# Performance work log

Measured on AMD Instinct MI355X. Metric: run time of the kernel, lower is better.

The kernel has to match this reference:

```python
import math
import jax, jax.numpy as jnp
import numpy as np

N_SENSORS = 4760
K = 16
HID = 64
D_LAT = 1024
D_PROJ = 128
POS_DIM = 96
FACE_DIM = 32
OUT_CH = 1
N_HEADS = 4
HEAD_DIM = D_PROJ // N_HEADS
N_TOKENS = 6
NUM_BANDS = POS_DIM // 6
B = 16


def _sinusoidal_pos_encoding(positions, num_bands):
    # positions: (N,3) numpy -> (N, num_bands*2*3)
    freq = (2.0 ** np.arange(num_bands, dtype=np.float32))
    encs = []
    for d in range(3):
        scaled = positions[:, d:d + 1] * freq[None, :] * (math.pi / 100.0)
        encs.append(np.sin(scaled))
        encs.append(np.cos(scaled))
    return np.concatenate(encs, axis=-1).astype(np.float32)


def setup_inputs() -> dict:
    rng = np.random.default_rng(0)
    positions = rng.uniform(-100.0, 100.0, (N_SENSORS, 3)).astype(np.float32)
    # kNN graph by 3D euclidean distance
    d2 = ((positions[:, None, :] - positions[None, :, :]) ** 2).sum(-1)
    knn = np.argsort(d2, axis=1)[:, :K].astype(np.int32)
    face_ids = rng.integers(0, 6, N_SENSORS).astype(np.int32)
    pos_embed = _sinusoidal_pos_encoding(positions, NUM_BANDS)  # (N,96)

    key = jax.random.key(0)
    ks = jax.random.split(key, 20)
    def lin(k, din, dout):
        k1, k2 = jax.random.split(k)
        lim = 1.0 / math.sqrt(din)
        W = jax.random.uniform(k1, (din, dout), jnp.float32, -lim, lim)
        b = jax.random.uniform(k2, (dout,), jnp.float32, -lim, lim)
        return W, b

    W_nbr, b_nbr = lin(ks[0], 2 + POS_DIM + FACE_DIM, HID)
    W_ql, b_ql = lin(ks[1], POS_DIM + FACE_DIM, HID)
    W_lat, b_lat = lin(ks[2], D_LAT, D_PROJ)
    W_lf, b_lf = lin(ks[3], FACE_DIM, D_PROJ)
    W_qg, b_qg = lin(ks[4], POS_DIM + FACE_DIM, D_PROJ)
    W_k, b_k = lin(ks[5], D_PROJ, D_PROJ)
    W_v, b_v = lin(ks[6], D_PROJ, D_PROJ)
    W_go, b_go = lin(ks[7], D_PROJ, D_PROJ)
    W_m1, b_m1 = lin(ks[8], HID + D_PROJ, HID)
    W_m2, b_m2 = lin(ks[9], HID, OUT_CH)
    face_emb = jax.random.normal(ks[10], (6, FACE_DIM), jnp.float32)
    ln_g = jnp.ones((HID + D_PROJ,), jnp.float32)
    ln_b = jnp.zeros((HID + D_PROJ,), jnp.float32)

    x_flat = jax.random.normal(ks[11], (B, N_SENSORS, 2), jnp.float32)
    latent_seq = jax.random.normal(ks[12], (B, N_TOKENS, D_LAT), jnp.float32)
    mask = jax.random.randint(ks[13], (B, N_SENSORS), 0, 2, jnp.int32)

    return dict(x_flat=x_flat, latent_seq=latent_seq, pos_embed=jnp.asarray(pos_embed),
                face_emb=face_emb, W_nbr=W_nbr, b_nbr=b_nbr, W_ql=W_ql, b_ql=b_ql,
                W_lat=W_lat, b_lat=b_lat, W_lf=W_lf, b_lf=b_lf, W_qg=W_qg, b_qg=b_qg,
                W_k=W_k, b_k=b_k, W_v=W_v, b_v=b_v, W_go=W_go, b_go=b_go,
                ln_g=ln_g, ln_b=ln_b, W_m1=W_m1, b_m1=b_m1, W_m2=W_m2, b_m2=b_m2,
                mask=mask, knn_indices=jnp.asarray(knn), face_ids=jnp.asarray(face_ids))


def _forward(x_flat, latent_seq, pos_embed, face_emb,
             W_nbr, b_nbr, W_ql, b_ql, W_lat, b_lat, W_lf, b_lf,
             W_qg, b_qg, W_k, b_k, W_v, b_v, W_go, b_go,
             ln_g, ln_b, W_m1, b_m1, W_m2, b_m2,
             mask, knn_indices, face_ids):
    # Dense equivalent: compute prediction for every (b, n), zero out unmasked.
    # query: (N, pos+face)
    query = jnp.concatenate([pos_embed, face_emb[face_ids]], axis=-1)  # (N,128)

    # ---- local kNN attention ----
    nbr_values = x_flat[:, knn_indices, :]                 # (B,N,K,2)
    nbr_pos = pos_embed[knn_indices]                       # (N,K,96)
    nbr_face = face_emb[face_ids[knn_indices]]             # (N,K,32)
    nbr_static = jnp.broadcast_to(
        jnp.concatenate([nbr_pos, nbr_face], axis=-1)[None],
        (x_flat.shape[0], N_SENSORS, K, POS_DIM + FACE_DIM))
    nbr_feat = jnp.concatenate([nbr_values, nbr_static], axis=-1)  # (B,N,K,130)
    nbr_feat = nbr_feat @ W_nbr + b_nbr                    # (B,N,K,H)

    nbr_is_masked = mask[:, knn_indices] != 0              # (B,N,K) bool
    q_local = query @ W_ql + b_ql                          # (N,H)
    scale = HID ** (-0.5)
    logits = jnp.einsum('bnkh,nh->bnk', nbr_feat, q_local) * scale
    logits = jnp.where(nbr_is_masked, -10000.0, logits)
    attn = jax.nn.softmax(logits, axis=-1)
    local_feat = jnp.einsum('bnk,bnkh->bnh', attn, nbr_feat)  # (B,N,H)

    # ---- global cross-attention over 6 latent tokens ----
    latent_p = latent_seq @ W_lat + b_lat                  # (B,T,P)
    face_bias = face_emb[jnp.arange(N_TOKENS)] @ W_lf + b_lf  # (T,P)
    latent_kv = latent_p + face_bias[None]                 # (B,T,P)
    q_g = (query @ W_qg + b_qg).reshape(N_SENSORS, N_HEADS, HEAD_DIM)
    k_g = (latent_kv @ W_k + b_k).reshape(-1, N_TOKENS, N_HEADS, HEAD_DIM)
    v_g = (latent_kv @ W_v + b_v).reshape(-1, N_TOKENS, N_HEADS, HEAD_DIM)
    g_logits = jnp.einsum('nhd,bthd->bnht', q_g, k_g) * (HEAD_DIM ** (-0.5))
    g_attn = jax.nn.softmax(g_logits, axis=-1)
    g_feat = jnp.einsum('bnht,bthd->bnhd', g_attn, v_g)
    g_feat = g_feat.reshape(-1, N_SENSORS, D_PROJ) @ W_go + b_go  # (B,N,P)

    # ---- prediction MLP: LayerNorm -> Linear -> GELU -> Linear ----
    combined = jnp.concatenate([local_feat, g_feat], axis=-1)  # (B,N,H+P)
    mu = combined.mean(-1, keepdims=True)
    var = combined.var(-1, keepdims=True)
    normed = (combined - mu) * jax.lax.rsqrt(var + 1e-5) * ln_g + ln_b
    h = jax.nn.gelu(normed @ W_m1 + b_m1, approximate=False)
    preds = h @ W_m2 + b_m2                                # (B,N,out)

    return preds * (mask != 0)[..., None].astype(preds.dtype)


def reference(x_flat, latent_seq, pos_embed, face_emb,
              W_nbr, b_nbr, W_ql, b_ql, W_lat, b_lat, W_lf, b_lf,
              W_qg, b_qg, W_k, b_k, W_v, b_v, W_go, b_go,
              ln_g, ln_b, W_m1, b_m1, W_m2, b_m2,
              mask, knn_indices, face_ids):
    return _forward(x_flat, latent_seq, pos_embed, face_emb,
                    W_nbr, b_nbr, W_ql, b_ql, W_lat, b_lat, W_lf, b_lf,
                    W_qg, b_qg, W_k, b_k, W_v, b_v, W_go, b_go,
                    ln_g, ln_b, W_m1, b_m1, W_m2, b_m2,
                    mask, knn_indices, face_ids)
```

## Files before the change

### kernel.cpp

```cpp
#include <hip/hip_runtime.h>
#include <math.h>

#define NSN 4760
#define KNN 16
#define NT 6
#define NB 16
#define NGB 595

__device__ __forceinline__ float rl_f(float v, int lane) {
  return __builtin_bit_cast(float, __builtin_amdgcn_readlane(__builtin_bit_cast(int, v), lane));
}

__global__ void precompute_sensor(const float* __restrict__ pos_emb,
    const float* __restrict__ face_emb, const int* __restrict__ face_ids,
    const float* __restrict__ W_nbr, const float* __restrict__ b_nbr,
    const float* __restrict__ W_ql, const float* __restrict__ b_ql,
    const float* __restrict__ W_qg, const float* __restrict__ b_qg,
    const float* __restrict__ W_m1, const float* __restrict__ ln_g,
    float* __restrict__ S, float* __restrict__ qlocal,
    float* __restrict__ qg, float* __restrict__ c01, float2* __restrict__ SS)
{
  __shared__ __align__(16) float qT[8][128][4];
  const int w = threadIdx.x >> 6, lane = threadIdx.x & 63;
  const int grp = blockIdx.x * 8 + w;
  if (grp >= NSN / 4) return;
  const int n0 = grp * 4;
  #pragma unroll
  for (int si = 0; si < 4; ++si) {
    const int n = n0 + si;
    const int fid = face_ids[n];
    const int e1 = lane + 64;
    qT[w][lane][si] = pos_emb[n * 96 + lane];
    qT[w][e1][si] = (e1 < 96) ? pos_emb[n * 96 + e1] : face_emb[fid * 32 + (e1 - 96)];
  }
  const float bn = b_nbr[lane], bq = b_ql[lane];
  const float bg0 = b_qg[lane], bg1 = b_qg[lane + 64];
  float s[4], ql[4], g0[4], g1[4];
  #pragma unroll
  for (int si = 0; si < 4; ++si) { s[si] = bn; ql[si] = bq; g0[si] = bg0; g1[si] = bg1; }
  #pragma unroll 2
  for (int i = 0; i < 128; ++i) {
    const float wn  = W_nbr[(2 + i) * 64 + lane];
    const float wq  = W_ql[i * 64 + lane];
    const float wg0 = W_qg[i * 128 + lane];
    const float wg1 = W_qg[i * 128 + 64 + lane];
    const float4 qv = *(const float4*)&qT[w][i][0];
    s[0]  += qv.x * wn;  s[1]  += qv.y * wn;  s[2]  += qv.z * wn;  s[3]  += qv.w * wn;
    ql[0] += qv.x * wq;  ql[1] += qv.y * wq;  ql[2] += qv.z * wq;  ql[3] += qv.w * wq;
    g0[0] += qv.x * wg0; g0[1] += qv.y * wg0; g0[2] += qv.z * wg0; g0[3] += qv.w * wg0;
    g1[0] += qv.x * wg1; g1[1] += qv.y * wg1; g1[2] += qv.z * wg1; g1[3] += qv.w * wg1;
  }
  const float wn0 = W_nbr[lane], wn1 = W_nbr[64 + lane];
  #pragma unroll
  for (int si = 0; si < 4; ++si) {
    const int n = n0 + si;
    S[n * 64 + lane] = s[si];
    qlocal[n * 64 + lane] = ql[si];
    qg[n * 128 + lane] = g0[si];
    qg[n * 128 + 64 + lane] = g1[si];
    float p0 = wn0 * ql[si], p1 = wn1 * ql[si];
    #pragma unroll
    for (int o = 32; o; o >>= 1) { p0 += __shfl_xor(p0, o); p1 += __shfl_xor(p1, o); }
    if (lane == 0) { c01[2 * n] = p0; c01[2 * n + 1] = p1; }
  }
  const float gl = ln_g[lane];
  #pragma unroll
  for (int si = 0; si < 4; ++si) qT[w][lane][si] = s[si] * gl;
  float sm0 = 0.f, sm1 = 0.f, sm2 = 0.f, sm3 = 0.f;
  #pragma unroll 4
  for (int h = 0; h < 64; ++h) {
    const float w1v = W_m1[h * 64 + lane];
    const float4 sv = *(const float4*)&qT[w][h][0];
    sm0 += sv.x * w1v; sm1 += sv.y * w1v; sm2 += sv.z * w1v; sm3 += sv.w * w1v;
  }
  SS[(n0 + 0) * 64 + lane] = make_float2(s[0], sm0);
  SS[(n0 + 1) * 64 + lane] = make_float2(s[1], sm1);
  SS[(n0 + 2) * 64 + lane] = make_float2(s[2], sm2);
  SS[(n0 + 3) * 64 + lane] = make_float2(s[3], sm3);
}

__global__ void precompute_latent(const float* __restrict__ latent,
    const float* __restrict__ face_emb,
    const float* __restrict__ W_lat, const float* __restrict__ b_lat,
    const float* __restrict__ W_lf, const float* __restrict__ b_lf,
    const float* __restrict__ W_k, const float* __restrict__ b_k,
    const float* __restrict__ W_v, const float* __restrict__ b_v,
    const float* __restrict__ W_go, const float* __restrict__ W_m1,
    const float* __restrict__ ln_g, const float* __restrict__ ln_b,
    const float* __restrict__ b_m1, const float* __restrict__ W_nbr,
    const float* __restrict__ b_go,
    float* __restrict__ kg, float4* __restrict__ TBL, float* __restrict__ C)
{
  const int bt = blockIdx.x;
  const int o = threadIdx.x;
  if (bt == NB * NT) {
    if (o < 64) {
      float wa = 0.f, wb = 0.f;
      #pragma unroll 4
      for (int h = 0; h < 64; ++h) {
        const float gw = ln_g[h] * W_m1[h * 64 + o];
        wa += W_nbr[h] * gw;
        wb += W_nbr[64 + h] * gw;
      }
      C[o] = wa; C[64 + o] = wb;
      float g = 0.f, p = 0.f;
      #pragma unroll 4
      for (int d = 0; d < 192; ++d) {
        const float w1 = W_m1[d * 64 + o];
        g += ln_g[d] * w1;
        p += ln_b[d] * w1;
      }
      C[128 + o] = g; C[192 + o] = p + b_m1[o];
      float c1 = 0.f;
      #pragma unroll 4
      for (int i = 0; i < 128; ++i)
        c1 += b_go[i] * ln_g[64 + i] * W_m1[(64 + i) * 64 + o];
      C[256 + o] = c1;
    }
    return;
  }
  __shared__ __align__(16) float lat[1024];
  __shared__ __align__(16) float kv[128];
  __shared__ __align__(16) float vrow[128];
  __shared__ __align__(16) float vwl[4][128];
  __shared__ __align__(16) float ghl[128];
  const int t = bt % NT;
  for (int i = o; i < 1024; i += 128) lat[i] = latent[bt * 1024 + i];
  ghl[o] = ln_g[64 + o];
  __syncthreads();
  float acc = b_lat[o] + b_lf[o];
  #pragma unroll 8
  for (int i = 0; i < 1024; ++i) acc += lat[i] * W_lat[i * 128 + o];
  #pragma unroll
  for (int i = 0; i < 32; ++i) acc += face_emb[t * 32 + i] * W_lf[i * 128 + o];
  kv[o] = acc;
  __syncthreads();
  float kk = b_k[o], vv = b_v[o];
  #pragma unroll 4
  for (int i = 0; i < 128; ++i) {
    const float c = kv[i];
    kk += c * W_k[i * 128 + o];
    vv += c * W_v[i * 128 + o];
  }
  kg[bt * 128 + o] = kk;
  vrow[o] = vv;
  __syncthreads();
  #pragma unroll
  for (int h = 0; h < 4; ++h) {
    float a = 0.f;
    #pragma unroll 8
    for (int i = 0; i < 32; ++i)
      a += vrow[h * 32 + i] * W_go[(h * 32 + i) * 128 + o];
    vwl[h][o] = a;
  }
  __syncthreads();
  if (o < 64) {
    #pragma unroll
    for (int h = 0; h < 4; ++h) {
      float m = 0.f;
      #pragma unroll 4
      for (int i = 0; i < 128; ++i)
        m += vwl[h][i] * ghl[i] * W_m1[(64 + i) * 64 + o];
      TBL[(bt * 4 + h) * 64 + o] =
          make_float4(vwl[h][2 * o], vwl[h][2 * o + 1], m, 0.f);
    }
  }
}

__launch_bounds__(512, 2)
__global__ void fused_main(const float* __restrict__ x_flat,
    const int* __restrict__ mask, const int* __restrict__ knn,
    const float* __restrict__ Wnbr,
    const float* __restrict__ S, const float* __restrict__ qlocal,
    const float* __restrict__ qg, const float* __restrict__ c01,
    const float* __restrict__ kg, const float2* __restrict__ SS,
    const float4* __restrict__ TBL, const float* __restrict__ CONSTS,
    const float* __restrict__ bgo, const float* __restrict__ Wm2,
    const float* __restrict__ bm2, float* __restrict__ out)
{
  __shared__ __align__(16) float4 TBLl[NT * 4 * 64];
  __shared__ __align__(16) float kgl[NT * 128];
  __shared__ __align__(16) float qlS[8][64];

  const int tid = threadIdx.x;
  const int b = blockIdx.x / NGB;
  const int ng = blockIdx.x - b * NGB;

  {
    const float4* tb = TBL + b * (NT * 4 * 64);
    for (int i = tid; i < NT * 4 * 64; i += 512) TBLl[i] = tb[i];
    const float* kgb = kg + b * (NT * 128);
    for (int i = tid; i < NT * 128; i += 512) kgl[i] = kgb[i];
  }
  __syncthreads();

  const int w = tid >> 6, lane = tid & 63;
  const int n = ng * 8 + w;
  const int item = b * NSN + n;

  const float wa  = CONSTS[lane],       wbc = CONSTS[64 + lane];
  const float cg  = CONSTS[128 + lane], cp  = CONSTS[192 + lane];
  const float cc1 = CONSTS[256 + lane];
  const float w0 = Wnbr[lane], w1 = Wnbr[64 + lane];
  const float bgo0 = bgo[2 * lane], bgo1 = bgo[2 * lane + 1];
  const float wm2 = Wm2[lane], bm2s = bm2[0];
  const float c0 = c01[2 * n], c1 = c01[2 * n + 1];
  const int mself = mask[item];

  const float ql = qlocal[n * 64 + lane];
  qlS[w][lane] = ql;
  int jv = 0, mk = 0; float x0 = 0.f, x1 = 0.f;
  if (lane < 16) {
    jv = knn[n * 16 + lane];
    const float2 x01 = *(const float2*)(x_flat + (size_t)(b * NSN + jv) * 2);
    x0 = x01.x; x1 = x01.y;
    mk = mask[b * NSN + jv];
  }

  const int k = lane >> 2, d = lane & 3;
  const int jk = __shfl(jv, k);
  const float4* Sr = (const float4*)(S + jk * 64 + d * 16);
  const float4* qr = (const float4*)(&qlS[w][d * 16]);
  float acc = 0.f;
  #pragma unroll
  for (int i = 0; i < 4; ++i) {
    const float4 sv = Sr[i]; const float4 qv = qr[i];
    acc += sv.x * qv.x + sv.y * qv.y + sv.z * qv.z + sv.w * qv.w;
  }
  acc += __shfl_xor(acc, 1); acc += __shfl_xor(acc, 2);
  const float xk0 = __shfl(x0, k), xk1 = __shfl(x1, k);
  const int mkk = __shfl(mk, k);
  float logit = (acc + xk0 * c0 + xk1 * c1) * 0.125f;
  if (mkk != 0) logit = -10000.0f;
  float mx = logit;
  mx = fmaxf(mx, __shfl_xor(mx, 4));  mx = fmaxf(mx, __shfl_xor(mx, 8));
  mx = fmaxf(mx, __shfl_xor(mx, 16)); mx = fmaxf(mx, __shfl_xor(mx, 32));
  const float e = __expf(logit - mx);
  float s4 = e;
  s4 += __shfl_xor(s4, 4); s4 += __shfl_xor(s4, 8);
  s4 += __shfl_xor(s4, 16); s4 += __shfl_xor(s4, 32);
  const float attn = e / s4;
  float ax0 = attn * xk0, ax1 = attn * xk1;
  ax0 += __shfl_xor(ax0, 4); ax0 += __shfl_xor(ax0, 8);
  ax0 += __shfl_xor(ax0, 16); ax0 += __shfl_xor(ax0, 32);
  ax1 += __shfl_xor(ax1, 4); ax1 += __shfl_xor(ax1, 8);
  ax1 += __shfl_xor(ax1, 16); ax1 += __shfl_xor(ax1, 32);

  float lf = ax0 * w0 + ax1 * w1;
  float L  = ax0 * wa + ax1 * wbc;
  #pragma unroll 4
  for (int kk = 0; kk < 16; ++kk) {
    const int jr = __builtin_amdgcn_readlane(jv, kk);
    const float aw = rl_f(attn, 4 * kk);
    const float2 ss = SS[jr * 64 + lane];
    lf += aw * ss.x;
    L  += aw * ss.y;
  }

  const float2 q2 = *(const float2*)(qg + n * 128 + 2 * lane);
  float av[NT];
  #pragma unroll
  for (int t = 0; t < NT; ++t) {
    const float2 k2 = *(const float2*)&kgl[t * 128 + 2 * lane];
    float p = q2.x * k2.x + q2.y * k2.y;
    p += __shfl_xor(p, 1); p += __shfl_xor(p, 2);
    p += __shfl_xor(p, 4); p += __shfl_xor(p, 8);
    av[t] = p * 0.17677669529663687f;
  }
  float gm = av[0];
  #pragma unroll
  for (int t = 1; t < NT; ++t) gm = fmaxf(gm, av[t]);
  float gs = 0.f;
  #pragma unroll
  for (int t = 0; t < NT; ++t) { av[t] = __expf(av[t] - gm); gs += av[t]; }
  const float ginv = 1.0f / gs;
  #pragma unroll
  for (int t = 0; t < NT; ++t) av[t] *= ginv;

  float g0 = bgo0, g1 = bgo1, M = 0.f;
  #pragma unroll 2
  for (int t = 0; t < NT; ++t) {
    #pragma unroll
    for (int h = 0; h < 4; ++h) {
      const float a = rl_f(av[t], 16 * h);
      const float4 tb = TBLl[(t * 4 + h) * 64 + lane];
      g0 += a * tb.x; g1 += a * tb.y; M += a * tb.z;
    }
  }

  float s1 = lf + g0 + g1;
  float s2 = lf * lf + g0 * g0 + g1 * g1;
  #pragma unroll
  for (int o = 32; o; o >>= 1) { s1 += __shfl_xor(s1, o); s2 += __shfl_xor(s2, o); }
  const float mu  = s1 * (1.0f / 192.0f);
  const float var = s2 * (1.0f / 192.0f) - mu * mu;
  const float rinv = rsqrtf(var + 1e-5f);

  const float m1 = rinv * (L + M + cc1 - mu * cg) + cp;
  const float gelu = 0.5f * m1 * (1.0f + erff(m1 * 0.7071067811865476f));
  float pr = gelu * wm2;
  #pragma unroll
  for (int o = 32; o; o >>= 1) pr += __shfl_xor(pr, o);
  float res = pr + bm2s;
  if (mself == 0) res = 0.f;
  if (lane == 0) out[item] = res;
}

extern "C" void kernel_launch(void* const* d_in, const int* in_sizes, int n_in,
                              void* d_out, int out_size, void* d_ws, size_t ws_size,
                              hipStream_t stream) {
  (void)in_sizes; (void)n_in; (void)out_size; (void)ws_size;
  const float* x_flat   = (const float*)d_in[0];
  const float* latent   = (const float*)d_in[1];
  const float* pos_emb  = (const float*)d_in[2];
  const float* face_emb = (const float*)d_in[3];
  const float* W_nbr = (const float*)d_in[4];
  const float* b_nbr = (const float*)d_in[5];
  const float* W_ql  = (const float*)d_in[6];
  const float* b_ql  = (const float*)d_in[7];
  const float* W_lat = (const float*)d_in[8];
  const float* b_lat = (const float*)d_in[9];
  const float* W_lf  = (const float*)d_in[10];
  const float* b_lf  = (const float*)d_in[11];
  const float* W_qg  = (const float*)d_in[12];
  const float* b_qg  = (const float*)d_in[13];
  const float* W_k   = (const float*)d_in[14];
  const float* b_k   = (const float*)d_in[15];
  const float* W_v   = (const float*)d_in[16];
  const float* b_v   = (const float*)d_in[17];
  const float* W_go  = (const float*)d_in[18];
  const float* b_go  = (const float*)d_in[19];
  const float* ln_g  = (const float*)d_in[20];
  const float* ln_b  = (const float*)d_in[21];
  const float* W_m1  = (const float*)d_in[22];
  const float* b_m1  = (const float*)d_in[23];
  const float* W_m2  = (const float*)d_in[24];
  const float* b_m2  = (const float*)d_in[25];
  const int* mask     = (const int*)d_in[26];
  const int* knn      = (const int*)d_in[27];
  const int* face_ids = (const int*)d_in[28];
  float* out = (float*)d_out;

  float* ws = (float*)d_ws;
  float* S      = ws;  ws += NSN * 64;
  float* qlocal = ws;  ws += NSN * 64;
  float* qgb    = ws;  ws += NSN * 128;
  float* c01    = ws;  ws += NSN * 2;
  float2* SSt   = (float2*)ws;  ws += NSN * 64 * 2;
  float* kgb    = ws;  ws += NB * NT * 128;
  float4* TBLt  = (float4*)ws;  ws += NB * NT * 4 * 64 * 4;
  float* CONSTS = ws;  ws += 5 * 64;

  precompute_sensor<<<149, 512, 0, stream>>>(pos_emb, face_emb, face_ids,
      W_nbr, b_nbr, W_ql, b_ql, W_qg, b_qg, W_m1, ln_g,
      S, qlocal, qgb, c01, SSt);
  precompute_latent<<<NB * NT + 1, 128, 0, stream>>>(latent, face_emb,
      W_lat, b_lat, W_lf, b_lf, W_k, b_k, W_v, b_v, W_go, W_m1, ln_g,
      ln_b, b_m1, W_nbr, b_go, kgb, TBLt, CONSTS);
  fused_main<<<NB * NGB, 512, 0, stream>>>(x_flat, mask, knn, W_nbr,
      S, qlocal, qgb, c01, kgb, SSt, TBLt, CONSTS,
      b_go, W_m2, b_m2, out);
}
```

Measured before the change: 320.9 us.

## Merge precompute kernels and make main kernel persistent over sensor groups

```diff
diff --git a/kernel.cpp b/kernel.cpp
--- a/kernel.cpp
+++ b/kernel.cpp
@@ -6,94 +6,139 @@
 #define NT 6
 #define NB 16
 #define NGB 595
+#define NBLK 85
 
 __device__ __forceinline__ float rl_f(float v, int lane) {
   return __builtin_bit_cast(float, __builtin_amdgcn_readlane(__builtin_bit_cast(int, v), lane));
 }
 
-__global__ void precompute_sensor(const float* __restrict__ pos_emb,
+__global__ void precompute_all(const float* __restrict__ pos_emb,
     const float* __restrict__ face_emb, const int* __restrict__ face_ids,
     const float* __restrict__ W_nbr, const float* __restrict__ b_nbr,
     const float* __restrict__ W_ql, const float* __restrict__ b_ql,
     const float* __restrict__ W_qg, const float* __restrict__ b_qg,
-    const float* __restrict__ W_m1, const float* __restrict__ ln_g,
-    float* __restrict__ S, float* __restrict__ qlocal,
-    float* __restrict__ qg, float* __restrict__ c01, float2* __restrict__ SS)
-{
-  __shared__ __align__(16) float qT[8][128][4];
-  const int w = threadIdx.x >> 6, lane = threadIdx.x & 63;
-  const int grp = blockIdx.x * 8 + w;
-  if (grp >= NSN / 4) return;
-  const int n0 = grp * 4;
-  #pragma unroll
-  for (int si = 0; si < 4; ++si) {
-    const int n = n0 + si;
-    const int fid = face_ids[n];
-    const int e1 = lane + 64;
-    qT[w][lane][si] = pos_emb[n * 96 + lane];
-    qT[w][e1][si] = (e1 < 96) ? pos_emb[n * 96 + e1] : face_emb[fid * 32 + (e1 - 96)];
-  }
-  const float bn = b_nbr[lane], bq = b_ql[lane];
-  const float bg0 = b_qg[lane], bg1 = b_qg[lane + 64];
-  float s[4], ql[4], g0[4], g1[4];
-  #pragma unroll
-  for (int si = 0; si < 4; ++si) { s[si] = bn; ql[si] = bq; g0[si] = bg0; g1[si] = bg1; }
-  #pragma unroll 2
-  for (int i = 0; i < 128; ++i) {
-    const float wn  = W_nbr[(2 + i) * 64 + lane];
-    const float wq  = W_ql[i * 64 + lane];
-    const float wg0 = W_qg[i * 128 + lane];
-    const float wg1 = W_qg[i * 128 + 64 + lane];
-    const float4 qv = *(const float4*)&qT[w][i][0];
-    s[0]  += qv.x * wn;  s[1]  += qv.y * wn;  s[2]  += qv.z * wn;  s[3]  += qv.w * wn;
-    ql[0] += qv.x * wq;  ql[1] += qv.y * wq;  ql[2] += qv.z * wq;  ql[3] += qv.w * wq;
-    g0[0] += qv.x * wg0; g0[1] += qv.y * wg0; g0[2] += qv.z * wg0; g0[3] += qv.w * wg0;
-    g1[0] += qv.x * wg1; g1[1] += qv.y * wg1; g1[2] += qv.z * wg1; g1[3] += qv.w * wg1;
-  }
-  const float wn0 = W_nbr[lane], wn1 = W_nbr[64 + lane];
-  #pragma unroll
-  for (int si = 0; si < 4; ++si) {
-    const int n = n0 + si;
-    S[n * 64 + lane] = s[si];
-    qlocal[n * 64 + lane] = ql[si];
-    qg[n * 128 + lane] = g0[si];
-    qg[n * 128 + 64 + lane] = g1[si];
-    float p0 = wn0 * ql[si], p1 = wn1 * ql[si];
-    #pragma unroll
-    for (int o = 32; o; o >>= 1) { p0 += __shfl_xor(p0, o); p1 += __shfl_xor(p1, o); }
-    if (lane == 0) { c01[2 * n] = p0; c01[2 * n + 1] = p1; }
-  }
-  const float gl = ln_g[lane];
-  #pragma unroll
-  for (int si = 0; si < 4; ++si) qT[w][lane][si] = s[si] * gl;
-  float sm0 = 0.f, sm1 = 0.f, sm2 = 0.f, sm3 = 0.f;
-  #pragma unroll 4
-  for (int h = 0; h < 64; ++h) {
-    const float w1v = W_m1[h * 64 + lane];
-    const float4 sv = *(const float4*)&qT[w][h][0];
-    sm0 += sv.x * w1v; sm1 += sv.y * w1v; sm2 += sv.z * w1v; sm3 += sv.w * w1v;
-  }
-  SS[(n0 + 0) * 64 + lane] = make_float2(s[0], sm0);
-  SS[(n0 + 1) * 64 + lane] = make_float2(s[1], sm1);
-  SS[(n0 + 2) * 64 + lane] = make_float2(s[2], sm2);
-  SS[(n0 + 3) * 64 + lane] = make_float2(s[3], sm3);
-}
-
-__global__ void precompute_latent(const float* __restrict__ latent,
-    const float* __restrict__ face_emb,
+    const float* __restrict__ latent,
     const float* __restrict__ W_lat, const float* __restrict__ b_lat,
     const float* __restrict__ W_lf, const float* __restrict__ b_lf,
     const float* __restrict__ W_k, const float* __restrict__ b_k,
     const float* __restrict__ W_v, const float* __restrict__ b_v,
-    const float* __restrict__ W_go, const float* __restrict__ W_m1,
+    const float* __restrict__ W_go, const float* __restrict__ b_go,
+    const float* __restrict__ W_m1, const float* __restrict__ b_m1,
     const float* __restrict__ ln_g, const float* __restrict__ ln_b,
-    const float* __restrict__ b_m1, const float* __restrict__ W_nbr,
-    const float* __restrict__ b_go,
+    float* __restrict__ S, float* __restrict__ qlocal,
+    float* __restrict__ qg, float* __restrict__ c01, float2* __restrict__ SS,
     float* __restrict__ kg, float4* __restrict__ TBL, float* __restrict__ C)
 {
-  const int bt = blockIdx.x;
-  const int o = threadIdx.x;
-  if (bt == NB * NT) {
+  __shared__ __align__(16) float qT[8][128][4];
+  __shared__ __align__(16) float lat[4][1024];
+  __shared__ __align__(16) float kvS[4][128];
+  __shared__ __align__(16) float vrow[4][128];
+  __shared__ __align__(16) float vwl[4][4][128];
+  const int bid = blockIdx.x;
+  const int tid = threadIdx.x;
+
+  if (bid < 149) {
+    const int w = tid >> 6, lane = tid & 63;
+    const int grp = bid * 8 + w;
+    if (grp >= NSN / 4) return;
+    const int n0 = grp * 4;
+    #pragma unroll
+    for (int si = 0; si < 4; ++si) {
+      const int n = n0 + si;
+      const int fid = face_ids[n];
+      const int e1 = lane + 64;
+      qT[w][lane][si] = pos_emb[n * 96 + lane];
+      qT[w][e1][si] = (e1 < 96) ? pos_emb[n * 96 + e1] : face_emb[fid * 32 + (e1 - 96)];
+    }
+    const float bn = b_nbr[lane], bq = b_ql[lane];
+    const float bg0 = b_qg[lane], bg1 = b_qg[lane + 64];
+    float s[4], ql[4], g0[4], g1[4];
+    #pragma unroll
+    for (int si = 0; si < 4; ++si) { s[si] = bn; ql[si] = bq; g0[si] = bg0; g1[si] = bg1; }
+    #pragma unroll 2
+    for (int i = 0; i < 128; ++i) {
+      const float wn  = W_nbr[(2 + i) * 64 + lane];
+      const float wq  = W_ql[i * 64 + lane];
+      const float wg0 = W_qg[i * 128 + lane];
+      const float wg1 = W_qg[i * 128 + 64 + lane];
+      const float4 qv = *(const float4*)&qT[w][i][0];
+      s[0]  += qv.x * wn;  s[1]  += qv.y * wn;  s[2]  += qv.z * wn;  s[3]  += qv.w * wn;
+      ql[0] += qv.x * wq;  ql[1] += qv.y * wq;  ql[2] += qv.z * wq;  ql[3] += qv.w * wq;
+      g0[0] += qv.x * wg0; g0[1] += qv.y * wg0; g0[2] += qv.z * wg0; g0[3] += qv.w * wg0;
+      g1[0] += qv.x * wg1; g1[1] += qv.y * wg1; g1[2] += qv.z * wg1; g1[3] += qv.w * wg1;
+    }
+    const float wn0 = W_nbr[lane], wn1 = W_nbr[64 + lane];
+    #pragma unroll
+    for (int si = 0; si < 4; ++si) {
+      const int n = n0 + si;
+      S[n * 64 + lane] = s[si];
+      qlocal[n * 64 + lane] = ql[si];
+      qg[n * 128 + lane] = g0[si];
+      qg[n * 128 + 64 + lane] = g1[si];
+      float p0 = wn0 * ql[si], p1 = wn1 * ql[si];
+      #pragma unroll
+      for (int o = 32; o; o >>= 1) { p0 += __shfl_xor(p0, o); p1 += __shfl_xor(p1, o); }
+      if (lane == 0) { c01[2 * n] = p0; c01[2 * n + 1] = p1; }
+    }
+    const float gl = ln_g[lane];
+    #pragma unroll
+    for (int si = 0; si < 4; ++si) qT[w][lane][si] = s[si] * gl;
+    float sm0 = 0.f, sm1 = 0.f, sm2 = 0.f, sm3 = 0.f;
+    #pragma unroll 4
+    for (int h = 0; h < 64; ++h) {
+      const float w1v = W_m1[h * 64 + lane];
+      const float4 sv = *(const float4*)&qT[w][h][0];
+      sm0 += sv.x * w1v; sm1 += sv.y * w1v; sm2 += sv.z * w1v; sm3 += sv.w * w1v;
+    }
+    SS[(n0 + 0) * 64 + lane] = make_float2(s[0], sm0);
+    SS[(n0 + 1) * 64 + lane] = make_float2(s[1], sm1);
+    SS[(n0 + 2) * 64 + lane] = make_float2(s[2], sm2);
+    SS[(n0 + 3) * 64 + lane] = make_float2(s[3], sm3);
+  } else if (bid < 173) {
+    const int team = tid >> 7, o = tid & 127;
+    const int bt = (bid - 149) * 4 + team;
+    const int t = bt % NT;
+    for (int i = o; i < 1024; i += 128) lat[team][i] = latent[bt * 1024 + i];
+    __syncthreads();
+    float acc = b_lat[o] + b_lf[o];
+    #pragma unroll 8
+    for (int i = 0; i < 1024; ++i) acc += lat[team][i] * W_lat[i * 128 + o];
+    #pragma unroll
+    for (int i = 0; i < 32; ++i) acc += face_emb[t * 32 + i] * W_lf[i * 128 + o];
+    kvS[team][o] = acc;
+    __syncthreads();
+    float kk = b_k[o], vv = b_v[o];
+    #pragma unroll 4
+    for (int i = 0; i < 128; ++i) {
+      const float c = kvS[team][i];
+      kk += c * W_k[i * 128 + o];
+      vv += c * W_v[i * 128 + o];
+    }
+    kg[bt * 128 + o] = kk;
+    vrow[team][o] = vv;
+    __syncthreads();
+    #pragma unroll
+    for (int h = 0; h < 4; ++h) {
+      float a = 0.f;
+      #pragma unroll 8
+      for (int i = 0; i < 32; ++i)
+        a += vrow[team][h * 32 + i] * W_go[(h * 32 + i) * 128 + o];
+      vwl[team][h][o] = a;
+    }
+    __syncthreads();
+    if (o < 64) {
+      #pragma unroll
+      for (int h = 0; h < 4; ++h) {
+        float m = 0.f;
+        #pragma unroll 4
+        for (int i = 0; i < 128; ++i)
+          m += vwl[team][h][i] * ln_g[64 + i] * W_m1[(64 + i) * 64 + o];
+        TBL[(bt * 4 + h) * 64 + o] =
+            make_float4(vwl[team][h][2 * o], vwl[team][h][2 * o + 1], m, 0.f);
+      }
+    }
+  } else {
+    const int o = tid;
     if (o < 64) {
       float wa = 0.f, wb = 0.f;
       #pragma unroll 4
@@ -117,53 +162,6 @@
         c1 += b_go[i] * ln_g[64 + i] * W_m1[(64 + i) * 64 + o];
       C[256 + o] = c1;
     }
-    return;
-  }
-  __shared__ __align__(16) float lat[1024];
-  __shared__ __align__(16) float kv[128];
-  __shared__ __align__(16) float vrow[128];
-  __shared__ __align__(16) float vwl[4][128];
-  __shared__ __align__(16) float ghl[128];
-  const int t = bt % NT;
-  for (int i = o; i < 1024; i += 128) lat[i] = latent[bt * 1024 + i];
-  ghl[o] = ln_g[64 + o];
-  __syncthreads();
-  float acc = b_lat[o] + b_lf[o];
-  #pragma unroll 8
-  for (int i = 0; i < 1024; ++i) acc += lat[i] * W_lat[i * 128 + o];
-  #pragma unroll
-  for (int i = 0; i < 32; ++i) acc += face_emb[t * 32 + i] * W_lf[i * 128 + o];
-  kv[o] = acc;
-  __syncthreads();
-  float kk = b_k[o], vv = b_v[o];
-  #pragma unroll 4
-  for (int i = 0; i < 128; ++i) {
-    const float c = kv[i];
-    kk += c * W_k[i * 128 + o];
-    vv += c * W_v[i * 128 + o];
-  }
-  kg[bt * 128 + o] = kk;
-  vrow[o] = vv;
-  __syncthreads();
-  #pragma unroll
-  for (int h = 0; h < 4; ++h) {
-    float a = 0.f;
-    #pragma unroll 8
-    for (int i = 0; i < 32; ++i)
-      a += vrow[h * 32 + i] * W_go[(h * 32 + i) * 128 + o];
-    vwl[h][o] = a;
-  }
-  __syncthreads();
-  if (o < 64) {
-    #pragma unroll
-    for (int h = 0; h < 4; ++h) {
-      float m = 0.f;
-      #pragma unroll 4
-      for (int i = 0; i < 128; ++i)
-        m += vwl[h][i] * ghl[i] * W_m1[(64 + i) * 64 + o];
-      TBL[(bt * 4 + h) * 64 + o] =
-          make_float4(vwl[h][2 * o], vwl[h][2 * o + 1], m, 0.f);
-    }
   }
 }
 
@@ -183,8 +181,8 @@
   __shared__ __align__(16) float qlS[8][64];
 
   const int tid = threadIdx.x;
-  const int b = blockIdx.x / NGB;
-  const int ng = blockIdx.x - b * NGB;
+  const int b = blockIdx.x / NBLK;
+  const int bg = blockIdx.x - b * NBLK;
 
   {
     const float4* tb = TBL + b * (NT * 4 * 64);
@@ -195,115 +193,134 @@
   __syncthreads();
 
   const int w = tid >> 6, lane = tid & 63;
-  const int n = ng * 8 + w;
-  const int item = b * NSN + n;
 
   const float wa  = CONSTS[lane],       wbc = CONSTS[64 + lane];
   const float cg  = CONSTS[128 + lane], cp  = CONSTS[192 + lane];
   const float cc1 = CONSTS[256 + lane];
   const float w0 = Wnbr[lane], w1 = Wnbr[64 + lane];
-  const float bgo0 = bgo[2 * lane], bgo1 = bgo[2 * lane + 1];
+  const float2 bgov = *(const float2*)(bgo + 2 * lane);
   const float wm2 = Wm2[lane], bm2s = bm2[0];
-  const float c0 = c01[2 * n], c1 = c01[2 * n + 1];
-  const int mself = mask[item];
-
-  const float ql = qlocal[n * 64 + lane];
-  qlS[w][lane] = ql;
-  int jv = 0, mk = 0; float x0 = 0.f, x1 = 0.f;
-  if (lane < 16) {
-    jv = knn[n * 16 + lane];
-    const float2 x01 = *(const float2*)(x_flat + (size_t)(b * NSN + jv) * 2);
-    x0 = x01.x; x1 = x01.y;
-    mk = mask[b * NSN + jv];
+
+  for (int ng = bg; ng < NGB; ng += NBLK) {
+    const int n = ng * 8 + w;
+    const int item = b * NSN + n;
+
+    const float2 c01v = *(const float2*)(c01 + 2 * n);
+    const int mself = mask[item];
+    const float ql = qlocal[n * 64 + lane];
+    const float2 q2 = *(const float2*)(qg + n * 128 + 2 * lane);
+    int jv = 0, mk = 0; float x0 = 0.f, x1 = 0.f;
+    if (lane < 16) {
+      jv = knn[n * 16 + lane];
+      const float2 x01 = *(const float2*)(x_flat + (size_t)(b * NSN + jv) * 2);
+      x0 = x01.x; x1 = x01.y;
+      mk = mask[b * NSN + jv];
+    }
+    qlS[w][lane] = ql;
+
+    const int k = lane >> 2, d = lane & 3;
+    const int jk = __shfl(jv, k);
+    const float4* Sr = (const float4*)(S + jk * 64 + d * 16);
+    const float4* qr = (const float4*)(&qlS[w][d * 16]);
+    float acc = 0.f;
+    #pragma unroll
+    for (int i = 0; i < 4; ++i) {
+      const float4 sv = Sr[i]; const float4 qv = qr[i];
+      acc += sv.x * qv.x + sv.y * qv.y + sv.z * qv.z + sv.w * qv.w;
+    }
+    acc += __shfl_xor(acc, 1); acc += __shfl_xor(acc, 2);
+    const float xk0 = __shfl(x0, k), xk1 = __shfl(x1, k);
+    const int mkk = __shfl(mk, k);
+    float logit = (acc + xk0 * c01v.x + xk1 * c01v.y) * 0.125f;
+    if (mkk != 0) logit = -10000.0f;
+    float mx = logit;
+    mx = fmaxf(mx, __shfl_xor(mx, 4));  mx = fmaxf(mx, __shfl_xor(mx, 8));
+    mx = fmaxf(mx, __shfl_xor(mx, 16)); mx = fmaxf(mx, __shfl_xor(mx, 32));
+    const float e = __expf(logit - mx);
+    float s4 = e;
+    s4 += __shfl_xor(s4, 4); s4 += __shfl_xor(s4, 8);
+    s4 += __shfl_xor(s4, 16); s4 += __shfl_xor(s4, 32);
+    const float attn = e / s4;
+    float ax0 = attn * xk0, ax1 = attn * xk1;
+    ax0 += __shfl_xor(ax0, 4); ax0 += __shfl_xor(ax0, 8);
+    ax0 += __shfl_xor(ax0, 16); ax0 += __shfl_xor(ax0, 32);
+    ax1 += __shfl_xor(ax1, 4); ax1 += __shfl_xor(ax1, 8);
+    ax1 += __shfl_xor(ax1, 16); ax1 += __shfl_xor(ax1, 32);
+
+    float lf = ax0 * w0 + ax1 * w1;
+    float L  = ax0 * wa + ax1 * wbc;
+    #pragma unroll
+    for (int kb = 0; kb < 4; ++kb) {
+      const int j0 = __builtin_amdgcn_readlane(jv, 4 * kb + 0);
+      const int j1 = __builtin_amdgcn_readlane(jv, 4 * kb + 1);
+      const int j2 = __builtin_amdgcn_readlane(jv, 4 * kb + 2);
+      const int j3 = __builtin_amdgcn_readlane(jv, 4 * kb + 3);
+      const float a0 = rl_f(attn, 16 * kb + 0);
+      const float a1 = rl_f(attn, 16 * kb + 4);
+      const float a2 = rl_f(attn, 16 * kb + 8);
+      const float a3 = rl_f(attn, 16 * kb + 12);
+      const float2 s0 = SS[j0 * 64 + lane];
+      const float2 s1 = SS[j1 * 64 + lane];
+      const float2 s2 = SS[j2 * 64 + lane];
+      const float2 s3 = SS[j3 * 64 + lane];
+      lf += a0 * s0.x + a1 * s1.x + a2 * s2.x + a3 * s3.x;
+      L  += a0 * s0.y + a1 * s1.y + a2 * s2.y + a3 * s3.y;
+    }
+
+    float2 k2v[NT];
+    #pragma unroll
+    for (int t = 0; t < NT; ++t) k2v[t] = *(const float2*)&kgl[t * 128 + 2 * lane];
+    float av[NT];
+    #pragma unroll
+    for (int t = 0; t < NT; ++t) {
+      float p = q2.x * k2v[t].x + q2.y * k2v[t].y;
+      p += __shfl_xor(p, 1); p += __shfl_xor(p, 2);
+      p += __shfl_xor(p, 4); p += __shfl_xor(p, 8);
+      av[t] = p * 0.17677669529663687f;
+    }
+    float gm = av[0];
+    #pragma unroll
+    for (int t = 1; t < NT; ++t) gm = fmaxf(gm, av[t]);
+    float gs = 0.f;
+    #pragma unroll
+    for (int t = 0; t < NT; ++t) { av[t] = __expf(av[t] - gm); gs += av[t]; }
+    const float ginv = 1.0f / gs;
+    #pragma unroll
+    for (int t = 0; t < NT; ++t) av[t] *= ginv;
+
+    float g0 = bgov.x, g1 = bgov.y, M = 0.f;
+    #pragma unroll
+    for (int t = 0; t < NT; ++t) {
+      const float4 r0 = TBLl[(t * 4 + 0) * 64 + lane];
+      const float4 r1 = TBLl[(t * 4 + 1) * 64 + lane];
+      const float4 r2 = TBLl[(t * 4 + 2) * 64 + lane];
+      const float4 r3 = TBLl[(t * 4 + 3) * 64 + lane];
+      const float a0 = rl_f(av[t], 0);
+      const float a1 = rl_f(av[t], 16);
+      const float a2 = rl_f(av[t], 32);
+      const float a3 = rl_f(av[t], 48);
+      g0 += a0 * r0.x + a1 * r1.x + a2 * r2.x + a3 * r3.x;
+      g1 += a0 * r0.y + a1 * r1.y + a2 * r2.y + a3 * r3.y;
+      M  += a0 * r0.z + a1 * r1.z + a2 * r2.z + a3 * r3.z;
+    }
+
+    float s1 = lf + g0 + g1;
+    float s2 = lf * lf + g0 * g0 + g1 * g1;
+    #pragma unroll
+    for (int o = 32; o; o >>= 1) { s1 += __shfl_xor(s1, o); s2 += __shfl_xor(s2, o); }
+    const float mu  = s1 * (1.0f / 192.0f);
+    const float var = s2 * (1.0f / 192.0f) - mu * mu;
+    const float rinv = rsqrtf(var + 1e-5f);
+
+    const float m1 = rinv * (L + M + cc1 - mu * cg) + cp;
+    const float gelu = 0.5f * m1 * (1.0f + erff(m1 * 0.7071067811865476f));
+    float pr = gelu * wm2;
+    #pragma unroll
+    for (int o = 32; o; o >>= 1) pr += __shfl_xor(pr, o);
+    float res = pr + bm2s;
+    if (mself == 0) res = 0.f;
+    if (lane == 0) out[item] = res;
   }
-
-  const int k = lane >> 2, d = lane & 3;
-  const int jk = __shfl(jv, k);
-  const float4* Sr = (const float4*)(S + jk * 64 + d * 16);
-  const float4* qr = (const float4*)(&qlS[w][d * 16]);
-  float acc = 0.f;
-  #pragma unroll
-  for (int i = 0; i < 4; ++i) {
-    const float4 sv = Sr[i]; const float4 qv = qr[i];
-    acc += sv.x * qv.x + sv.y * qv.y + sv.z * qv.z + sv.w * qv.w;
-  }
-  acc += __shfl_xor(acc, 1); acc += __shfl_xor(acc, 2);
-  const float xk0 = __shfl(x0, k), xk1 = __shfl(x1, k);
-  const int mkk = __shfl(mk, k);
-  float logit = (acc + xk0 * c0 + xk1 * c1) * 0.125f;
-  if (mkk != 0) logit = -10000.0f;
-  float mx = logit;
-  mx = fmaxf(mx, __shfl_xor(mx, 4));  mx = fmaxf(mx, __shfl_xor(mx, 8));
-  mx = fmaxf(mx, __shfl_xor(mx, 16)); mx = fmaxf(mx, __shfl_xor(mx, 32));
-  const float e = __expf(logit - mx);
-  float s4 = e;
-  s4 += __shfl_xor(s4, 4); s4 += __shfl_xor(s4, 8);
-  s4 += __shfl_xor(s4, 16); s4 += __shfl_xor(s4, 32);
-  const float attn = e / s4;
-  float ax0 = attn * xk0, ax1 = attn * xk1;
-  ax0 += __shfl_xor(ax0, 4); ax0 += __shfl_xor(ax0, 8);
-  ax0 += __shfl_xor(ax0, 16); ax0 += __shfl_xor(ax0, 32);
-  ax1 += __shfl_xor(ax1, 4); ax1 += __shfl_xor(ax1, 8);
-  ax1 += __shfl_xor(ax1, 16); ax1 += __shfl_xor(ax1, 32);
-
-  float lf = ax0 * w0 + ax1 * w1;
-  float L  = ax0 * wa + ax1 * wbc;
-  #pragma unroll 4
-  for (int kk = 0; kk < 16; ++kk) {
-    const int jr = __builtin_amdgcn_readlane(jv, kk);
-    const float aw = rl_f(attn, 4 * kk);
-    const float2 ss = SS[jr * 64 + lane];
-    lf += aw * ss.x;
-    L  += aw * ss.y;
-  }
-
-  const float2 q2 = *(const float2*)(qg + n * 128 + 2 * lane);
-  float av[NT];
-  #pragma unroll
-  for (int t = 0; t < NT; ++t) {
-    const float2 k2 = *(const float2*)&kgl[t * 128 + 2 * lane];
-    float p = q2.x * k2.x + q2.y * k2.y;
-    p += __shfl_xor(p, 1); p += __shfl_xor(p, 2);
-    p += __shfl_xor(p, 4); p += __shfl_xor(p, 8);
-    av[t] = p * 0.17677669529663687f;
-  }
-  float gm = av[0];
-  #pragma unroll
-  for (int t = 1; t < NT; ++t) gm = fmaxf(gm, av[t]);
-  float gs = 0.f;
-  #pragma unroll
-  for (int t = 0; t < NT; ++t) { av[t] = __expf(av[t] - gm); gs += av[t]; }
-  const float ginv = 1.0f / gs;
-  #pragma unroll
-  for (int t = 0; t < NT; ++t) av[t] *= ginv;
-
-  float g0 = bgo0, g1 = bgo1, M = 0.f;
-  #pragma unroll 2
-  for (int t = 0; t < NT; ++t) {
-    #pragma unroll
-    for (int h = 0; h < 4; ++h) {
-      const float a = rl_f(av[t], 16 * h);
-      const float4 tb = TBLl[(t * 4 + h) * 64 + lane];
-      g0 += a * tb.x; g1 += a * tb.y; M += a * tb.z;
-    }
-  }
-
-  float s1 = lf + g0 + g1;
-  float s2 = lf * lf + g0 * g0 + g1 * g1;
-  #pragma unroll
-  for (int o = 32; o; o >>= 1) { s1 += __shfl_xor(s1, o); s2 += __shfl_xor(s2, o); }
-  const float mu  = s1 * (1.0f / 192.0f);
-  const float var = s2 * (1.0f / 192.0f) - mu * mu;
-  const float rinv = rsqrtf(var + 1e-5f);
-
-  const float m1 = rinv * (L + M + cc1 - mu * cg) + cp;
-  const float gelu = 0.5f * m1 * (1.0f + erff(m1 * 0.7071067811865476f));
-  float pr = gelu * wm2;
-  #pragma unroll
-  for (int o = 32; o; o >>= 1) pr += __shfl_xor(pr, o);
-  float res = pr + bm2s;
-  if (mself == 0) res = 0.f;
-  if (lane == 0) out[item] = res;
 }
 
 extern "C" void kernel_launch(void* const* d_in, const int* in_sizes, int n_in,
@@ -351,13 +368,12 @@
   float4* TBLt  = (float4*)ws;  ws += NB * NT * 4 * 64 * 4;
   float* CONSTS = ws;  ws += 5 * 64;
 
-  precompute_sensor<<<149, 512, 0, stream>>>(pos_emb, face_emb, face_ids,
-      W_nbr, b_nbr, W_ql, b_ql, W_qg, b_qg, W_m1, ln_g,
-      S, qlocal, qgb, c01, SSt);
-  precompute_latent<<<NB * NT + 1, 128, 0, stream>>>(latent, face_emb,
-      W_lat, b_lat, W_lf, b_lf, W_k, b_k, W_v, b_v, W_go, W_m1, ln_g,
-      ln_b, b_m1, W_nbr, b_go, kgb, TBLt, CONSTS);
-  fused_main<<<NB * NGB, 512, 0, stream>>>(x_flat, mask, knn, W_nbr,
+  precompute_all<<<174, 512, 0, stream>>>(pos_emb, face_emb, face_ids,
+      W_nbr, b_nbr, W_ql, b_ql, W_qg, b_qg,
+      latent, W_lat, b_lat, W_lf, b_lf, W_k, b_k, W_v, b_v,
+      W_go, b_go, W_m1, b_m1, ln_g, ln_b,
+      S, qlocal, qgb, c01, SSt, kgb, TBLt, CONSTS);
+  fused_main<<<NB * NBLK, 512, 0, stream>>>(x_flat, mask, knn, W_nbr,
       S, qlocal, qgb, c01, kgb, SSt, TBLt, CONSTS,
       b_go, W_m2, b_m2, out);
 }
```

Measured after the change: 412.0 us. 28.4% more time.
